# Performance work log

Hardware: AMD Instinct MI355X
Metric: run time of the kernel (lower is better)

## Reference

```python
import jax, jax.numpy as jnp
import numpy as np

N = 50000      # nodes
E = 800000     # edges (avg degree 16)
F_IN = 128
# (d_in, d_out) for the 9 GCNConv layers with width=256, n_layers=3
DIMS = [(128, 128), (128, 192), (192, 256), (256, 256), (256, 256), (256, 256), (256, 192), (192, 128), (128, 1)]
# ReLU after every conv except loop conv i==n_layers-2 (conv idx 4) and the final conv
RELU = [True, True, True, True, False, True, True, True, False]


def setup_inputs() -> dict:
    key = jax.random.key(0)
    ks = jax.random.split(key, 2 + 2 * len(DIMS))
    inp = {
        "x": jax.random.normal(ks[0], (N, F_IN), dtype=jnp.float32),
        "edge_index": jax.random.randint(ks[1], (2, E), 0, N, dtype=jnp.int64),
    }
    for i, (din, dout) in enumerate(DIMS):
        # Glorot-ish init for weights, small random bias (GCNConv has bias=True)
        inp[f"W{i}"] = jax.random.normal(ks[2 + 2 * i], (din, dout), dtype=jnp.float32) / np.float32(np.sqrt(din))
        inp[f"b{i}"] = jax.random.normal(ks[3 + 2 * i], (dout,), dtype=jnp.float32) * 0.01
    return inp


def _gcn_stack(x, src_f, dst_f, norm, Ws, bs):
    h = x
    for i in range(len(Ws)):
        h = h @ Ws[i]                                  # [N, dout] dense transform first (dout <= din mostly)
        msg = h[src_f] * norm[:, None]                 # gather + edge-normalize  [E+N, dout]
        h = jax.ops.segment_sum(msg, dst_f, num_segments=N) + bs[i]
        if RELU[i]:
            h = jax.nn.relu(h)
        # Dropout layers are identity in eval/inference mode.
    return h


def reference(x, edge_index,
              W0, b0, W1, b1, W2, b2, W3, b3, W4, b4, W5, b5, W6, b6, W7, b7, W8, b8):
    src, dst = edge_index[0], edge_index[1]
    loop = jnp.arange(N, dtype=src.dtype)
    # GCNConv default: add self loops, symmetric normalization D^{-1/2}(A+I)D^{-1/2}
    src_f = jnp.concatenate([src, loop])
    dst_f = jnp.concatenate([dst, loop])
    deg = jax.ops.segment_sum(jnp.ones(E + N, dtype=x.dtype), dst_f, num_segments=N)
    dinv = jax.lax.rsqrt(jnp.maximum(deg, 1.0))        # deg >= 1 thanks to self loops
    norm = dinv[src_f] * dinv[dst_f]                   # per-edge coefficient [E+N]
    Ws = [W0, W1, W2, W3, W4, W5, W6, W7, W8]
    bs = [b0, b1, b2, b3, b4, b5, b6, b7, b8]
    return _gcn_stack(x, src_f, dst_f, norm, Ws, bs)   # [N, 1]
```

## Files before the change

### kernel.cpp

```cpp
#include <hip/hip_runtime.h>


#define TPB 256

using bf16x8 = __attribute__((ext_vector_type(8))) __bf16;
using f32x4  = __attribute__((ext_vector_type(4))) float;
using f32x2  = __attribute__((ext_vector_type(2))) float;

__device__ __forceinline__ unsigned bf16rne(float x) {
    unsigned u = __float_as_uint(x);
    return (u + 0x7fffu + ((u >> 16) & 1u)) >> 16;
}

__device__ __forceinline__ f32x2 bl2(unsigned u) {
    return (f32x2){__uint_as_float(u << 16), __uint_as_float(u & 0xffff0000u)};
}

__device__ __forceinline__ void stage16(const unsigned short* g, unsigned short* l) {
#if __has_builtin(__builtin_amdgcn_global_load_lds)
    __builtin_amdgcn_global_load_lds((const __attribute__((address_space(1))) void*)g,
                                     (__attribute__((address_space(3))) void*)l, 16, 0, 0);
#else
    *(uint4*)((char*)l + (threadIdx.x & 63) * 16) = *(const uint4*)g;
#endif
}


__global__ void count_kernel(const int* __restrict__ dst, int* __restrict__ cnt,
                             int* __restrict__ rank, int E) {
    int e = blockIdx.x * blockDim.x + threadIdx.x;
    if (e < E) rank[e] = atomicAdd(&cnt[dst[e]], 1);
}


__global__ void blockhist_kernel(const int* __restrict__ cnt, int* __restrict__ localRank,
                                 int* __restrict__ hb, float* __restrict__ dinv,
                                 int n, int nb) {
    __shared__ int h[64];
    int t = threadIdx.x;
    if (t < 64) h[t] = 0;
    __syncthreads();
    int i = blockIdx.x * TPB + t;
    if (i < n) {
        int c = cnt[i];
        dinv[i] = rsqrtf((float)(c + 1));
        int d = c; if (d > 63) d = 63;
        localRank[i] = atomicAdd(&h[d], 1);
    }
    __syncthreads();
    if (t < 64) hb[t * nb + blockIdx.x] = h[t];
}

__global__ __launch_bounds__(256) void sortscan_kernel(int* __restrict__ hb, int nb) {
    __shared__ int sh[64 * 256];
    __shared__ int qs[64 * 4];
    __shared__ int tot[64], base[64];
    int t = threadIdx.x;
    int total = 64 * nb;
    for (int i = t; i < total; i += 256) sh[i] = hb[i];
    __syncthreads();
    int bin = t >> 2, qt = t & 3;
    int nq = (nb + 3) >> 2;
    int c0 = qt * nq, c1 = c0 + nq; if (c1 > nb) c1 = nb;
    int run = 0;
    for (int b = c0; b < c1; b++) {
        int v = sh[bin * nb + b];
        sh[bin * nb + b] = run;
        run += v;
    }
    qs[bin * 4 + qt] = run;
    __syncthreads();
    if (qt == 0) {
        int acc = 0;
#pragma unroll
        for (int q = 0; q < 4; q++) { int v = qs[bin * 4 + q]; qs[bin * 4 + q] = acc; acc += v; }
        tot[bin] = acc;
    }
    __syncthreads();
    if (t == 0) {
        int acc = 0;
        for (int b = 0; b < 64; b++) { base[b] = acc; acc += tot[b]; }
    }
    __syncthreads();
    int add = qs[bin * 4 + qt];
    for (int b = c0; b < c1; b++) sh[bin * nb + b] += add;
    __syncthreads();
    for (int i = t; i < total; i += 256) hb[i] = sh[i] + base[i / nb];
}

__global__ void scatter2_kernel(const int* __restrict__ cnt,
                                const int* __restrict__ localRank, const int* __restrict__ hb,
                                int* __restrict__ perm, int* __restrict__ pcnt,
                                int* __restrict__ iperm, int n, int nb) {
    int i = blockIdx.x * TPB + threadIdx.x;
    if (i >= n) return;
    int c = cnt[i];
    int d = c; if (d > 63) d = 63;
    int pos = hb[d * nb + blockIdx.x] + localRank[i];
    perm[pos] = i;
    pcnt[pos] = c;
    iperm[i] = pos;
}

__global__ void scan1_kernel(const int* __restrict__ pcnt, int* __restrict__ prowp2,
                             int* __restrict__ bsums, int n) {
    __shared__ int sh[TPB];
    int t = threadIdx.x;
    int i = blockIdx.x * TPB + t;
    int v = (i < n) ? (pcnt[i] + 1) : 0;
    sh[t] = v;
    __syncthreads();
    for (int off = 1; off < TPB; off <<= 1) {
        int x = (t >= off) ? sh[t - off] : 0;
        __syncthreads();
        sh[t] += x;
        __syncthreads();
    }
    if (i < n) prowp2[i] = sh[t] - v;
    if (t == TPB - 1) bsums[blockIdx.x] = sh[t];
}

__global__ void scan3_kernel(int* __restrict__ rowp, const int* __restrict__ bsums,
                             int n, int nb) {
    __shared__ int sh[TPB];
    int t = threadIdx.x;
    int v = (t < nb && t < (int)blockIdx.x) ? bsums[t] : 0;
    sh[t] = v;
    __syncthreads();
    for (int off = 1; off < TPB; off <<= 1) {
        int x = (t >= off) ? sh[t - off] : 0;
        __syncthreads();
        sh[t] += x;
        __syncthreads();
    }
    int offset = sh[TPB - 1];
    int i = blockIdx.x * TPB + t;
    if (i < n) rowp[i] += offset;
}

__global__ void rowo_kernel(const int* __restrict__ iperm, const int* __restrict__ prowp2,
                            const float* __restrict__ dinv, int2* __restrict__ rd, int n) {
    int i = blockIdx.x * TPB + threadIdx.x;
    if (i < n) rd[i] = make_int2(prowp2[iperm[i]], __float_as_int(dinv[i]));
}

__global__ void fillself_kernel(const int* __restrict__ src, const int* __restrict__ dst,
                                const int* __restrict__ rank,
                                const float* __restrict__ dinv,
                                const int2* __restrict__ rd,
                                const int* __restrict__ cnt,
                                unsigned* __restrict__ edges2, int E, int n) {
    int id = blockIdx.x * blockDim.x + threadIdx.x;
    if (id < E) {
        int s = src[id], d = dst[id];
        int2 rv = rd[d];
        int pos = rv.x + rank[id];
        edges2[pos] = (unsigned)s | (bf16rne(dinv[s] * __int_as_float(rv.y)) << 16);
    } else if (id < E + n) {
        int i = id - E;
        int2 rv = rd[i];
        float dv = __int_as_float(rv.y);
        edges2[rv.x + cnt[i]] = (unsigned)i | (bf16rne(dv * dv) << 16);
    }
}


struct WPtrs { const float* p[8]; };

__global__ void wtcvt_kernel(WPtrs wp, unsigned short* __restrict__ Wts,
                             const float* __restrict__ xin,
                             unsigned short* __restrict__ Bx, int n4,
                             int* __restrict__ cnt, int n) {
    const int cum[9] = {0, 16384, 40960, 90112, 155648, 221184, 286720, 335872, 360448};
    const int Ns[8] = {128, 192, 256, 256, 256, 256, 192, 128};
    const int Ks[8] = {128, 128, 192, 256, 256, 256, 256, 192};
    int id = blockIdx.x * blockDim.x + threadIdx.x;
    if (id < 360448) {
        int L = 0;
#pragma unroll
        for (int t = 1; t < 8; t++) if (id >= cum[t]) L = t;
        int lid = id - cum[L];
        int N = Ns[L], K = Ks[L];
        int k = lid / N, n2 = lid - k * N;
        Wts[cum[L] + n2 * K + k] = (unsigned short)bf16rne(wp.p[L][lid]);
    } else if (id < 360448 + n4) {
        int i = id - 360448;
        float4 v = ((const float4*)xin)[i];
        uint2 o;
        o.x = bf16rne(v.x) | (bf16rne(v.y) << 16);
        o.y = bf16rne(v.z) | (bf16rne(v.w) << 16);
        ((uint2*)Bx)[i] = o;
    } else {
        int i = id - 360448 - n4;
        if (i < n) cnt[i] = 0;
    }
}


template<int NFR>
__global__ __launch_bounds__(512, 4) void gemm2_kernel(
    const unsigned short* __restrict__ A, const unsigned short* __restrict__ Wt,
    const float* __restrict__ bias, unsigned short* __restrict__ C,
    int M, int K, int doBias, int doRelu, int outChunked) {
    constexpr int Nc = NFR * 64;
    __shared__ unsigned short Qb[2][128 * 32];
    __shared__ unsigned short Pb[2][Nc * 32];
    int tid = threadIdx.x;
    int l = tid & 63, w = tid >> 6;
    int node0 = blockIdx.x * 128;

    f32x4 acc[4][NFR];
#pragma unroll
    for (int j = 0; j < 4; j++)
#pragma unroll
        for (int f = 0; f < NFR; f++) acc[j][f] = (f32x4){0.f, 0.f, 0.f, 0.f};

    int rA = tid >> 2, qA = tid & 3;
    int nd = node0 + rA; if (nd > M - 1) nd = M - 1;
    const unsigned short* gA = A + (size_t)nd * K + (qA ^ (rA & 3)) * 8;
    const unsigned short* gW0 = Wt + (size_t)rA * K + (qA ^ (rA & 3)) * 8;
    const unsigned short* gW1 = gW0;
    if (NFR >= 3) {
        int rW1 = 128 + rA;
        gW1 = Wt + (size_t)rW1 * K + (qA ^ (rW1 & 3)) * 8;
    }
    int lB = w * 512;

    int q4 = l >> 4, m16 = l & 15;
    int nodeHalf = w >> 2, fq = w & 3;
    int rQ0 = nodeHalf * 64 + m16;
    int rP0 = fq * (NFR * 16) + m16;
    int swq8 = (q4 ^ (m16 & 3)) * 8;
    int nk = K >> 5;

    {
        stage16(gA, Qb[0] + lB);
        stage16(gW0, Pb[0] + lB);
        if constexpr (NFR == 4) stage16(gW1, Pb[0] + 4096 + lB);
        else if constexpr (NFR == 3) { if (w < 4) stage16(gW1, Pb[0] + 4096 + lB); }
    }
    __syncthreads();

    int cur = 0;
    for (int t = 0; t < nk; t++) {
        if (t + 1 < nk) {
            int k0 = (t + 1) << 5;
            stage16(gA + k0, Qb[cur ^ 1] + lB);
            stage16(gW0 + k0, Pb[cur ^ 1] + lB);
            if constexpr (NFR == 4) stage16(gW1 + k0, Pb[cur ^ 1] + 4096 + lB);
            else if constexpr (NFR == 3) { if (w < 4) stage16(gW1 + k0, Pb[cur ^ 1] + 4096 + lB); }
        }
        bf16x8 qf[4], pf[NFR];
#pragma unroll
        for (int j = 0; j < 4; j++)
            qf[j] = *(const bf16x8*)(Qb[cur] + (rQ0 + j * 16) * 32 + swq8);
#pragma unroll
        for (int f = 0; f < NFR; f++)
            pf[f] = *(const bf16x8*)(Pb[cur] + (rP0 + f * 16) * 32 + swq8);
#pragma unroll
        for (int j = 0; j < 4; j++)
#pragma unroll
            for (int f = 0; f < NFR; f++)
                acc[j][f] = __builtin_amdgcn_mfma_f32_16x16x32_bf16(pf[f], qf[j],
                                                                    acc[j][f], 0, 0, 0);
        __syncthreads();
        cur ^= 1;
    }

#pragma unroll
    for (int f = 0; f < NFR; f++) {
        int gf0 = fq * (NFR * 16) + f * 16 + q4 * 4;
        float4 bv = make_float4(0.f, 0.f, 0.f, 0.f);
        if (doBias) bv = *(const float4*)(bias + gf0);
        size_t cb = outChunked ? ((size_t)(gf0 >> 6) * ((size_t)M * 64) + (gf0 & 63))
                               : (size_t)gf0;
#pragma unroll
        for (int j = 0; j < 4; j++) {
            int gn = node0 + nodeHalf * 64 + j * 16 + m16;
            if (gn >= M) continue;
            f32x4 v = acc[j][f];
            float x0 = v[0] + bv.x, x1 = v[1] + bv.y;
            float x2 = v[2] + bv.z, x3 = v[3] + bv.w;
            if (doRelu) {
                x0 = fmaxf(x0, 0.f); x1 = fmaxf(x1, 0.f);
                x2 = fmaxf(x2, 0.f); x3 = fmaxf(x3, 0.f);
            }
            uint2 o;
            o.x = bf16rne(x0) | (bf16rne(x1) << 16);
            o.y = bf16rne(x2) | (bf16rne(x3) << 16);
            size_t off = outChunked ? (cb + (size_t)gn * 64) : (cb + (size_t)gn * Nc);
            *(uint2*)(C + off) = o;
        }
    }
}

__global__ void gemv128_bf16_kernel(const unsigned short* __restrict__ A,
                                    const float* __restrict__ w,
                                    float* __restrict__ out, int M) {
    int wid = (blockIdx.x * blockDim.x + threadIdx.x) >> 6;
    int lane = threadIdx.x & 63;
    if (wid >= M) return;
    const unsigned short* a = A + (size_t)wid * 128;
    float a0 = __uint_as_float((unsigned)a[lane] << 16);
    float a1 = __uint_as_float((unsigned)a[lane + 64] << 16);
    float s = a0 * w[lane] + a1 * w[lane + 64];
#pragma unroll
    for (int off = 32; off > 0; off >>= 1) s += __shfl_down(s, off);
    if (lane == 0) out[wid] = s;
}


__global__ __launch_bounds__(256) void agg_group_kernel(
    const uint4* __restrict__ in, const int* __restrict__ prowp2,
    const int* __restrict__ pcnt, const int* __restrict__ perm,
    const unsigned* __restrict__ edges2,
    const float* __restrict__ bias, uint4* __restrict__ out,
    int Q, int upx, int ngPerUnit, int NG, int n_nodes, int rowVec4,
    int doBias, int doRelu, int outChunked) {
    int xcd = blockIdx.x & 7;
    int slot = blockIdx.x >> 3;
    int u = slot / ngPerUnit;
    int ngIdx = slot - u * ngPerUnit;
    int unit = xcd * upx + u;
    int chunk = unit / Q;
    int q = unit - chunk * Q;
    int ng = ngIdx * Q + q;
    if (ng >= NG) return;
    ng = NG - 1 - ng;

    int wave = threadIdx.x >> 6;
    int lane = threadIdx.x & 63;
    int group = lane >> 3, fl = lane & 7;
    int gb = lane & ~7;
    int i = ng * 32 + wave * 8 + group;
    if (i >= n_nodes) return;

    const uint4* sf = in + (size_t)chunk * n_nodes * 8 + fl;
    int s0 = prowp2[i];
    int c = pcnt[i] + 1;
    int node = perm[i];
    const unsigned* ep = edges2 + s0;

    f32x2 acc[2][4];
#pragma unroll
    for (int k = 0; k < 2; k++)
#pragma unroll
        for (int m = 0; m < 4; m++) acc[k][m] = (f32x2){0.f, 0.f};

    unsigned ew = (fl < c) ? ep[fl] : 0u;
    unsigned eA[4]; uint4 pA[4];
#pragma unroll
    for (int j = 0; j < 4; j++) eA[j] = (unsigned)__shfl((int)ew, gb + j);
#pragma unroll
    for (int j = 0; j < 4; j++) pA[j] = sf[(size_t)(eA[j] & 0xffffu) * 8];

    for (int base = 0; base < c; base += 8) {
        unsigned ewn = (base + 8 + fl < c) ? ep[base + 8 + fl] : 0u;
        unsigned eB[4]; uint4 pB[4];
#pragma unroll
        for (int j = 0; j < 4; j++) eB[j] = (unsigned)__shfl((int)ew, gb + 4 + j);
#pragma unroll
        for (int j = 0; j < 4; j++) pB[j] = sf[(size_t)(eB[j] & 0xffffu) * 8];
#pragma unroll
        for (int j = 0; j < 4; j++) {
            float wgt = __uint_as_float(eA[j] & 0xffff0000u);
            f32x2 w2 = {wgt, wgt};
            int k = j & 1;
            acc[k][0] += w2 * bl2(pA[j].x);
            acc[k][1] += w2 * bl2(pA[j].y);
            acc[k][2] += w2 * bl2(pA[j].z);
            acc[k][3] += w2 * bl2(pA[j].w);
        }
#pragma unroll
        for (int j = 0; j < 4; j++) eA[j] = (unsigned)__shfl((int)ewn, gb + j);
#pragma unroll
        for (int j = 0; j < 4; j++) pA[j] = sf[(size_t)(eA[j] & 0xffffu) * 8];
#pragma unroll
        for (int j = 0; j < 4; j++) {
            float wgt = __uint_as_float(eB[j] & 0xffff0000u);
            f32x2 w2 = {wgt, wgt};
            int k = j & 1;
            acc[k][0] += w2 * bl2(pB[j].x);
            acc[k][1] += w2 * bl2(pB[j].y);
            acc[k][2] += w2 * bl2(pB[j].z);
            acc[k][3] += w2 * bl2(pB[j].w);
        }
        ew = ewn;
    }
    f32x2 s[4];
#pragma unroll
    for (int m = 0; m < 4; m++) s[m] = acc[0][m] + acc[1][m];

    if (doBias) {
        const float* bp = bias + chunk * 64 + fl * 8;
        float4 b0 = *(const float4*)bp;
        float4 b1 = *(const float4*)(bp + 4);
        s[0] += (f32x2){b0.x, b0.y};
        s[1] += (f32x2){b0.z, b0.w};
        s[2] += (f32x2){b1.x, b1.y};
        s[3] += (f32x2){b1.z, b1.w};
    }
    if (doRelu) {
#pragma unroll
        for (int m = 0; m < 4; m++) {
            s[m][0] = fmaxf(s[m][0], 0.f);
            s[m][1] = fmaxf(s[m][1], 0.f);
        }
    }
    uint4 o;
    o.x = bf16rne(s[0][0]) | (bf16rne(s[0][1]) << 16);
    o.y = bf16rne(s[1][0]) | (bf16rne(s[1][1]) << 16);
    o.z = bf16rne(s[2][0]) | (bf16rne(s[2][1]) << 16);
    o.w = bf16rne(s[3][0]) | (bf16rne(s[3][1]) << 16);
    size_t oi = outChunked ? ((size_t)chunk * n_nodes * 8 + (size_t)node * 8 + fl)
                           : ((size_t)node * rowVec4 + chunk * 8 + fl);
    out[oi] = o;
}

__global__ void agg1_kernel(const float* __restrict__ in, const int* __restrict__ prowp2,
                            const int* __restrict__ pcnt, const int* __restrict__ perm,
                            const unsigned* __restrict__ edges2,
                            const float* __restrict__ bias, float* __restrict__ out,
                            int n_nodes) {
    int n = blockIdx.x * blockDim.x + threadIdx.x;
    if (n >= n_nodes) return;
    float acc = 0.f;
    int s0 = prowp2[n];
    int c = pcnt[n] + 1;
    for (int j = 0; j < c; j++) {
        unsigned e = edges2[s0 + j];
        acc += __uint_as_float(e & 0xffff0000u) * in[e & 0xffffu];
    }
    acc += bias[0];
    out[perm[n]] = acc;
}


extern "C" void kernel_launch(void* const* d_in, const int* in_sizes, int n_in,
                              void* d_out, int out_size, void* d_ws, size_t ws_size,
                              hipStream_t stream) {
    const float* x = (const float*)d_in[0];
    const int* ei = (const int*)d_in[1];
    const int Nn = in_sizes[0] / 128;
    const int E = in_sizes[1] / 2;
    const int* src = ei;
    const int* dst = ei + E;

    char* ws = (char*)d_ws;
    size_t off = 0;
    auto alloc = [&](size_t bytes) -> char* {
        char* p = ws + off;
        off = (off + bytes + 255) & ~(size_t)255;
        return p;
    };
    int* cnt = (int*)alloc((size_t)Nn * 4);
    int* rank = (int*)alloc((size_t)E * 4);
    int* bsums = (int*)alloc(1024);
    float* dinv = (float*)alloc((size_t)Nn * 4);
    int* localRank = (int*)alloc((size_t)Nn * 4);
    int* hb = (int*)alloc((size_t)64 * 256 * 4);
    int* perm = (int*)alloc((size_t)Nn * 4);
    int* pcnt = (int*)alloc((size_t)Nn * 4);
    int* iperm = (int*)alloc((size_t)Nn * 4);
    int* prowp2 = (int*)alloc((size_t)Nn * 4);
    int2* rd = (int2*)alloc((size_t)Nn * 8);
    unsigned* edges2 = (unsigned*)alloc((size_t)(E + Nn + 64) * 4);
    unsigned short* T = (unsigned short*)alloc((size_t)Nn * 256 * 2);
    unsigned short* H = (unsigned short*)alloc((size_t)Nn * 256 * 2);
    unsigned short* Bx = (unsigned short*)alloc((size_t)Nn * 128 * 2);
    float* F = (float*)alloc((size_t)Nn * 4);
    unsigned short* Wts = (unsigned short*)alloc((size_t)400000 * 2);
    (void)ws_size;

    const int dims[9][2] = {{128,128},{128,192},{192,256},{256,256},{256,256},
                            {256,256},{256,192},{192,128},{128,1}};
    unsigned short* Wt[8];
    {
        size_t o = 0;
        for (int i = 0; i < 8; i++) { Wt[i] = Wts + o; o += (size_t)dims[i][0] * dims[i][1]; }
    }

    int nbN = (Nn + TPB - 1) / TPB;
    int nbE = (E + TPB - 1) / TPB;
    int nbEN = (E + Nn + TPB - 1) / TPB;

    WPtrs wp;
    for (int i = 0; i < 8; i++) wp.p[i] = (const float*)d_in[2 + 2 * i];
    int n4 = Nn * 32;
    wtcvt_kernel<<<(360448 + n4 + Nn + TPB - 1) / TPB, TPB, 0, stream>>>(
        wp, Wts, x, Bx, n4, cnt, Nn);

    count_kernel<<<nbE, TPB, 0, stream>>>(dst, cnt, rank, E);
    blockhist_kernel<<<nbN, TPB, 0, stream>>>(cnt, localRank, hb, dinv, Nn, nbN);
    sortscan_kernel<<<1, 256, 0, stream>>>(hb, nbN);
    scatter2_kernel<<<nbN, TPB, 0, stream>>>(cnt, localRank, hb, perm, pcnt, iperm,
                                             Nn, nbN);
    scan1_kernel<<<nbN, TPB, 0, stream>>>(pcnt, prowp2, bsums, Nn);
    scan3_kernel<<<nbN, TPB, 0, stream>>>(prowp2, bsums, Nn, nbN);
    rowo_kernel<<<nbN, TPB, 0, stream>>>(iperm, prowp2, dinv, rd, Nn);
    fillself_kernel<<<nbEN, TPB, 0, stream>>>(src, dst, rank, dinv, rd, cnt,
                                              edges2, E, Nn);

    int ntx = (Nn + 127) / 128;
    auto gemm = [&](const unsigned short* A, int i, unsigned short* C, int K, int Nc,
                    int doBias, int doRelu, int outChunked) {
        const float* b = (const float*)d_in[3 + 2 * i];
        if (Nc == 256)
            gemm2_kernel<4><<<ntx, 512, 0, stream>>>(A, Wt[i], b, C, Nn, K,
                                                     doBias, doRelu, outChunked);
        else if (Nc == 192)
            gemm2_kernel<3><<<ntx, 512, 0, stream>>>(A, Wt[i], b, C, Nn, K,
                                                     doBias, doRelu, outChunked);
        else
            gemm2_kernel<2><<<ntx, 512, 0, stream>>>(A, Wt[i], b, C, Nn, K,
                                                     doBias, doRelu, outChunked);
    };
    int NG = (Nn + 31) / 32;
    auto agg = [&](const unsigned short* inb, unsigned short* outb, int w, int i,
                   int doBias, int doRelu, int outChunked) {
        int nch = w / 64;
        int Q = (nch == 4) ? 2 : (nch == 3) ? 8 : 4;
        int upx = nch * Q / 8;
        int ngPerUnit = (NG + Q - 1) / Q;
        int blocksPerXcd = upx * ngPerUnit;
        const float* b = (const float*)d_in[3 + 2 * i];
        agg_group_kernel<<<blocksPerXcd * 8, 256, 0, stream>>>(
            (const uint4*)inb, prowp2, pcnt, perm, edges2, b, (uint4*)outb,
            Q, upx, ngPerUnit, NG, Nn, w / 8, doBias, doRelu, outChunked);
    };

    gemm(Bx, 0, T, 128, 128, 0, 0, 1);
    agg(T, H, 128, 0, 1, 1, 1);
    agg(H, T, 128, 1, 0, 0, 0);
    gemm(T, 1, H, 128, 192, 1, 1, 1);
    agg(H, T, 192, 2, 0, 0, 0);
    gemm(T, 2, H, 192, 256, 1, 1, 0);
    gemm(H, 3, T, 256, 256, 0, 0, 1);
    agg(T, H, 256, 3, 1, 1, 0);
    gemm(H, 4, T, 256, 256, 0, 0, 1);
    agg(T, H, 256, 4, 1, 0, 0);
    gemm(H, 5, T, 256, 256, 0, 0, 1);
    agg(T, H, 256, 5, 1, 1, 0);
    gemm(H, 6, T, 256, 192, 0, 0, 1);
    agg(T, H, 192, 6, 1, 1, 0);
    gemm(H, 7, T, 192, 128, 0, 0, 1);
    agg(T, H, 128, 7, 1, 1, 0);
    gemv128_bf16_kernel<<<(Nn + 3) / 4, 256, 0, stream>>>(H, (const float*)d_in[2 + 16],
                                                          F, Nn);
    agg1_kernel<<<nbN, TPB, 0, stream>>>(F, prowp2, pcnt, perm, edges2,
                                         (const float*)d_in[3 + 16], (float*)d_out, Nn);
}
```

Measured before the change: 558.0 us.

## Partition each node's edge list by source half into two aggregated segments

During CSR construction each destination's incoming edges (plus its self loop) are split into two contiguous groups, sources in the low half of node ids and sources in the high half. The aggregation kernel then walks the two segments one after the other. The intent appears to be better cache locality for the feature gathers, since a wavefront first touches only the lower half of the feature table and then only the upper half. In exchange it adds a second count array, a wider per-node record and per-segment prologue and tail overhead in the aggregation loop, which matters because the average degree is small.

```diff
diff --git a/kernel.cpp b/kernel.cpp
--- a/kernel.cpp
+++ b/kernel.cpp
@@ -26,14 +26,20 @@
 }
 
 
-__global__ void count_kernel(const int* __restrict__ dst, int* __restrict__ cnt,
-                             int* __restrict__ rank, int E) {
+__global__ void count_kernel(const int* __restrict__ src, const int* __restrict__ dst,
+                             int* __restrict__ cnt2, int* __restrict__ rank,
+                             int E, int halfN, int n) {
     int e = blockIdx.x * blockDim.x + threadIdx.x;
-    if (e < E) rank[e] = atomicAdd(&cnt[dst[e]], 1);
-}
-
-
-__global__ void blockhist_kernel(const int* __restrict__ cnt, int* __restrict__ localRank,
+    if (e < E) {
+        int d = dst[e];
+        int half = (src[e] >= halfN) ? 1 : 0;
+        int rk = atomicAdd(&cnt2[d + half * n], 1);
+        rank[e] = rk | (half << 30);
+    }
+}
+
+
+__global__ void blockhist_kernel(const int* __restrict__ cnt2, int* __restrict__ localRank,
                                  int* __restrict__ hb, float* __restrict__ dinv,
                                  int n, int nb) {
     __shared__ int h[64];
@@ -42,7 +48,7 @@
     __syncthreads();
     int i = blockIdx.x * TPB + t;
     if (i < n) {
-        int c = cnt[i];
+        int c = cnt2[i] + cnt2[i + n];
         dinv[i] = rsqrtf((float)(c + 1));
         int d = c; if (d > 63) d = 63;
         localRank[i] = atomicAdd(&h[d], 1);
@@ -88,17 +94,20 @@
     for (int i = t; i < total; i += 256) hb[i] = sh[i] + base[i / nb];
 }
 
-__global__ void scatter2_kernel(const int* __restrict__ cnt,
+__global__ void scatter2_kernel(const int* __restrict__ cnt2,
                                 const int* __restrict__ localRank, const int* __restrict__ hb,
                                 int* __restrict__ perm, int* __restrict__ pcnt,
-                                int* __restrict__ iperm, int n, int nb) {
+                                int* __restrict__ pcl, int* __restrict__ iperm,
+                                int n, int nb, int halfN) {
     int i = blockIdx.x * TPB + threadIdx.x;
     if (i >= n) return;
-    int c = cnt[i];
+    int lo = cnt2[i];
+    int c = lo + cnt2[i + n];
     int d = c; if (d > 63) d = 63;
     int pos = hb[d * nb + blockIdx.x] + localRank[i];
     perm[pos] = i;
     pcnt[pos] = c;
+    pcl[pos] = lo + (i < halfN ? 1 : 0);
     iperm[i] = pos;
 }
 
@@ -138,29 +147,38 @@
     if (i < n) rowp[i] += offset;
 }
 
-__global__ void rowo_kernel(const int* __restrict__ iperm, const int* __restrict__ prowp2,
-                            const float* __restrict__ dinv, int2* __restrict__ rd, int n) {
+__global__ void rd4_kernel(const int* __restrict__ iperm, const int* __restrict__ prowp2,
+                           const float* __restrict__ dinv, const int* __restrict__ cnt2,
+                           int4* __restrict__ rd, int n, int halfN) {
     int i = blockIdx.x * TPB + threadIdx.x;
-    if (i < n) rd[i] = make_int2(prowp2[iperm[i]], __float_as_int(dinv[i]));
+    if (i >= n) return;
+    int lo = cnt2[i];
+    int tot = lo + cnt2[i + n];
+    int base = prowp2[iperm[i]];
+    bool selfLo = (i < halfN);
+    rd[i] = make_int4(base, __float_as_int(dinv[i]),
+                      base + lo + (selfLo ? 1 : 0),
+                      selfLo ? (base + lo) : (base + tot));
 }
 
 __global__ void fillself_kernel(const int* __restrict__ src, const int* __restrict__ dst,
                                 const int* __restrict__ rank,
                                 const float* __restrict__ dinv,
-                                const int2* __restrict__ rd,
-                                const int* __restrict__ cnt,
+                                const int4* __restrict__ rd,
                                 unsigned* __restrict__ edges2, int E, int n) {
     int id = blockIdx.x * blockDim.x + threadIdx.x;
     if (id < E) {
         int s = src[id], d = dst[id];
-        int2 rv = rd[d];
-        int pos = rv.x + rank[id];
+        int r = rank[id];
+        int rk = r & 0x3fffffff, half = r >> 30;
+        int4 rv = rd[d];
+        int pos = (half ? rv.z : rv.x) + rk;
         edges2[pos] = (unsigned)s | (bf16rne(dinv[s] * __int_as_float(rv.y)) << 16);
     } else if (id < E + n) {
         int i = id - E;
-        int2 rv = rd[i];
+        int4 rv = rd[i];
         float dv = __int_as_float(rv.y);
-        edges2[rv.x + cnt[i]] = (unsigned)i | (bf16rne(dv * dv) << 16);
+        edges2[rv.w] = (unsigned)i | (bf16rne(dv * dv) << 16);
     }
 }
 
@@ -170,7 +188,7 @@
 __global__ void wtcvt_kernel(WPtrs wp, unsigned short* __restrict__ Wts,
                              const float* __restrict__ xin,
                              unsigned short* __restrict__ Bx, int n4,
-                             int* __restrict__ cnt, int n) {
+                             int* __restrict__ cnt2, int n2) {
     const int cum[9] = {0, 16384, 40960, 90112, 155648, 221184, 286720, 335872, 360448};
     const int Ns[8] = {128, 192, 256, 256, 256, 256, 192, 128};
     const int Ks[8] = {128, 128, 192, 256, 256, 256, 256, 192};
@@ -181,8 +199,8 @@
         for (int t = 1; t < 8; t++) if (id >= cum[t]) L = t;
         int lid = id - cum[L];
         int N = Ns[L], K = Ks[L];
-        int k = lid / N, n2 = lid - k * N;
-        Wts[cum[L] + n2 * K + k] = (unsigned short)bf16rne(wp.p[L][lid]);
+        int k = lid / N, n = lid - k * N;
+        Wts[cum[L] + n * K + k] = (unsigned short)bf16rne(wp.p[L][lid]);
     } else if (id < 360448 + n4) {
         int i = id - 360448;
         float4 v = ((const float4*)xin)[i];
@@ -192,7 +210,7 @@
         ((uint2*)Bx)[i] = o;
     } else {
         int i = id - 360448 - n4;
-        if (i < n) cnt[i] = 0;
+        if (i < n2) cnt2[i] = 0;
     }
 }
 
@@ -312,8 +330,8 @@
 
 __global__ __launch_bounds__(256) void agg_group_kernel(
     const uint4* __restrict__ in, const int* __restrict__ prowp2,
-    const int* __restrict__ pcnt, const int* __restrict__ perm,
-    const unsigned* __restrict__ edges2,
+    const int* __restrict__ pcnt, const int* __restrict__ pcl,
+    const int* __restrict__ perm, const unsigned* __restrict__ edges2,
     const float* __restrict__ bias, uint4* __restrict__ out,
     int Q, int upx, int ngPerUnit, int NG, int n_nodes, int rowVec4,
     int doBias, int doRelu, int outChunked) {
@@ -338,8 +356,8 @@
     const uint4* sf = in + (size_t)chunk * n_nodes * 8 + fl;
     int s0 = prowp2[i];
     int c = pcnt[i] + 1;
+    int cl = pcl[i];
     int node = perm[i];
-    const unsigned* ep = edges2 + s0;
 
     f32x2 acc[2][4];
 #pragma unroll
@@ -347,46 +365,51 @@
 #pragma unroll
         for (int m = 0; m < 4; m++) acc[k][m] = (f32x2){0.f, 0.f};
 
-    unsigned ew = (fl < c) ? ep[fl] : 0u;
-    unsigned eA[4]; uint4 pA[4];
-#pragma unroll
-    for (int j = 0; j < 4; j++) eA[j] = (unsigned)__shfl((int)ew, gb + j);
-#pragma unroll
-    for (int j = 0; j < 4; j++) pA[j] = sf[(size_t)(eA[j] & 0xffffu) * 8];
-
-    for (int base = 0; base < c; base += 8) {
-        unsigned ewn = (base + 8 + fl < c) ? ep[base + 8 + fl] : 0u;
-        unsigned eB[4]; uint4 pB[4];
-#pragma unroll
-        for (int j = 0; j < 4; j++) eB[j] = (unsigned)__shfl((int)ew, gb + 4 + j);
-#pragma unroll
-        for (int j = 0; j < 4; j++) pB[j] = sf[(size_t)(eB[j] & 0xffffu) * 8];
-#pragma unroll
-        for (int j = 0; j < 4; j++) {
-            float wgt = __uint_as_float(eA[j] & 0xffff0000u);
-            f32x2 w2 = {wgt, wgt};
-            int k = j & 1;
-            acc[k][0] += w2 * bl2(pA[j].x);
-            acc[k][1] += w2 * bl2(pA[j].y);
-            acc[k][2] += w2 * bl2(pA[j].z);
-            acc[k][3] += w2 * bl2(pA[j].w);
+    auto seg = [&](const unsigned* p, int m) {
+        if (m <= 0) return;
+        unsigned ew = (fl < m) ? p[fl] : 0u;
+        unsigned eA[4]; uint4 pA[4];
+#pragma unroll
+        for (int j = 0; j < 4; j++) eA[j] = (unsigned)__shfl((int)ew, gb + j);
+#pragma unroll
+        for (int j = 0; j < 4; j++) pA[j] = sf[(size_t)(eA[j] & 0xffffu) * 8];
+        for (int base = 0; base < m; base += 8) {
+            unsigned ewn = (base + 8 + fl < m) ? p[base + 8 + fl] : 0u;
+            unsigned eB[4]; uint4 pB[4];
+#pragma unroll
+            for (int j = 0; j < 4; j++) eB[j] = (unsigned)__shfl((int)ew, gb + 4 + j);
+#pragma unroll
+            for (int j = 0; j < 4; j++) pB[j] = sf[(size_t)(eB[j] & 0xffffu) * 8];
+#pragma unroll
+            for (int j = 0; j < 4; j++) {
+                float wgt = __uint_as_float(eA[j] & 0xffff0000u);
+                f32x2 w2 = {wgt, wgt};
+                int k = j & 1;
+                acc[k][0] += w2 * bl2(pA[j].x);
+                acc[k][1] += w2 * bl2(pA[j].y);
+                acc[k][2] += w2 * bl2(pA[j].z);
+                acc[k][3] += w2 * bl2(pA[j].w);
+            }
+#pragma unroll
+            for (int j = 0; j < 4; j++) eA[j] = (unsigned)__shfl((int)ewn, gb + j);
+#pragma unroll
+            for (int j = 0; j < 4; j++) pA[j] = sf[(size_t)(eA[j] & 0xffffu) * 8];
+#pragma unroll
+            for (int j = 0; j < 4; j++) {
+                float wgt = __uint_as_float(eB[j] & 0xffff0000u);
+                f32x2 w2 = {wgt, wgt};
+                int k = j & 1;
+                acc[k][0] += w2 * bl2(pB[j].x);
+                acc[k][1] += w2 * bl2(pB[j].y);
+                acc[k][2] += w2 * bl2(pB[j].z);
+                acc[k][3] += w2 * bl2(pB[j].w);
+            }
+            ew = ewn;
         }
-#pragma unroll
-        for (int j = 0; j < 4; j++) eA[j] = (unsigned)__shfl((int)ewn, gb + j);
-#pragma unroll
-        for (int j = 0; j < 4; j++) pA[j] = sf[(size_t)(eA[j] & 0xffffu) * 8];
-#pragma unroll
-        for (int j = 0; j < 4; j++) {
-            float wgt = __uint_as_float(eB[j] & 0xffff0000u);
-            f32x2 w2 = {wgt, wgt};
-            int k = j & 1;
-            acc[k][0] += w2 * bl2(pB[j].x);
-            acc[k][1] += w2 * bl2(pB[j].y);
-            acc[k][2] += w2 * bl2(pB[j].z);
-            acc[k][3] += w2 * bl2(pB[j].w);
-        }
-        ew = ewn;
-    }
+    };
+    seg(edges2 + s0, cl);
+    seg(edges2 + s0 + cl, c - cl);
+
     f32x2 s[4];
 #pragma unroll
     for (int m = 0; m < 4; m++) s[m] = acc[0][m] + acc[1][m];
@@ -445,6 +468,7 @@
     const int E = in_sizes[1] / 2;
     const int* src = ei;
     const int* dst = ei + E;
+    const int halfN = Nn >> 1;
 
     char* ws = (char*)d_ws;
     size_t off = 0;
@@ -453,7 +477,7 @@
         off = (off + bytes + 255) & ~(size_t)255;
         return p;
     };
-    int* cnt = (int*)alloc((size_t)Nn * 4);
+    int* cnt2 = (int*)alloc((size_t)Nn * 8);
     int* rank = (int*)alloc((size_t)E * 4);
     int* bsums = (int*)alloc(1024);
     float* dinv = (float*)alloc((size_t)Nn * 4);
@@ -461,9 +485,10 @@
     int* hb = (int*)alloc((size_t)64 * 256 * 4);
     int* perm = (int*)alloc((size_t)Nn * 4);
     int* pcnt = (int*)alloc((size_t)Nn * 4);
+    int* pcl = (int*)alloc((size_t)Nn * 4);
     int* iperm = (int*)alloc((size_t)Nn * 4);
     int* prowp2 = (int*)alloc((size_t)Nn * 4);
-    int2* rd = (int2*)alloc((size_t)Nn * 8);
+    int4* rd = (int4*)alloc((size_t)Nn * 16);
     unsigned* edges2 = (unsigned*)alloc((size_t)(E + Nn + 64) * 4);
     unsigned short* T = (unsigned short*)alloc((size_t)Nn * 256 * 2);
     unsigned short* H = (unsigned short*)alloc((size_t)Nn * 256 * 2);
@@ -487,19 +512,18 @@
     WPtrs wp;
     for (int i = 0; i < 8; i++) wp.p[i] = (const float*)d_in[2 + 2 * i];
     int n4 = Nn * 32;
-    wtcvt_kernel<<<(360448 + n4 + Nn + TPB - 1) / TPB, TPB, 0, stream>>>(
-        wp, Wts, x, Bx, n4, cnt, Nn);
-
-    count_kernel<<<nbE, TPB, 0, stream>>>(dst, cnt, rank, E);
-    blockhist_kernel<<<nbN, TPB, 0, stream>>>(cnt, localRank, hb, dinv, Nn, nbN);
+    wtcvt_kernel<<<(360448 + n4 + 2 * Nn + TPB - 1) / TPB, TPB, 0, stream>>>(
+        wp, Wts, x, Bx, n4, cnt2, 2 * Nn);
+
+    count_kernel<<<nbE, TPB, 0, stream>>>(src, dst, cnt2, rank, E, halfN, Nn);
+    blockhist_kernel<<<nbN, TPB, 0, stream>>>(cnt2, localRank, hb, dinv, Nn, nbN);
     sortscan_kernel<<<1, 256, 0, stream>>>(hb, nbN);
-    scatter2_kernel<<<nbN, TPB, 0, stream>>>(cnt, localRank, hb, perm, pcnt, iperm,
-                                             Nn, nbN);
+    scatter2_kernel<<<nbN, TPB, 0, stream>>>(cnt2, localRank, hb, perm, pcnt, pcl,
+                                             iperm, Nn, nbN, halfN);
     scan1_kernel<<<nbN, TPB, 0, stream>>>(pcnt, prowp2, bsums, Nn);
     scan3_kernel<<<nbN, TPB, 0, stream>>>(prowp2, bsums, Nn, nbN);
-    rowo_kernel<<<nbN, TPB, 0, stream>>>(iperm, prowp2, dinv, rd, Nn);
-    fillself_kernel<<<nbEN, TPB, 0, stream>>>(src, dst, rank, dinv, rd, cnt,
-                                              edges2, E, Nn);
+    rd4_kernel<<<nbN, TPB, 0, stream>>>(iperm, prowp2, dinv, cnt2, rd, Nn, halfN);
+    fillself_kernel<<<nbEN, TPB, 0, stream>>>(src, dst, rank, dinv, rd, edges2, E, Nn);
 
     int ntx = (Nn + 127) / 128;
     auto gemm = [&](const unsigned short* A, int i, unsigned short* C, int K, int Nc,
@@ -525,7 +549,7 @@
         int blocksPerXcd = upx * ngPerUnit;
         const float* b = (const float*)d_in[3 + 2 * i];
         agg_group_kernel<<<blocksPerXcd * 8, 256, 0, stream>>>(
-            (const uint4*)inb, prowp2, pcnt, perm, edges2, b, (uint4*)outb,
+            (const uint4*)inb, prowp2, pcnt, pcl, perm, edges2, b, (uint4*)outb,
             Q, upx, ngPerUnit, NG, Nn, w / 8, doBias, doRelu, outChunked);
     };
 
```

Result: slower. 586.7 us (+5.1%).
